# Kernel tuning notes

Measured on AMD Instinct MI355X. Metric: run time of the kernel, lower is better.

## Reference

```python
import jax, jax.numpy as jnp
import numpy as np

OBS_DIM = 512
ACT_DIM = 32
HIDDEN_DIM = 1024
MSG_DIM = 128
POS_EM_DIM = 128
T = 256


def pos_table(n, dim):
    pos = np.arange(n)[:, None].astype(np.float64)
    j = np.arange(dim)[None, :]
    tab = pos / np.power(10000.0, 2 * (j // 2) / dim)
    tab[:, 0::2] = np.sin(tab[:, 0::2])
    tab[:, 1::2] = np.cos(tab[:, 1::2])
    return tab.astype(np.float32)


def setup_inputs() -> dict:
    key = jax.random.key(0)
    ks = jax.random.split(key, 12)
    in_dim = 1 + ACT_DIM
    s = 0.1
    return {
        "obs": jax.random.normal(ks[0], (T, OBS_DIM), jnp.float32),
        "prev_act": jax.random.normal(ks[1], (T, ACT_DIM), jnp.float32),
        "in_shift": jnp.zeros((OBS_DIM,), jnp.float32),
        "in_scale": jnp.ones((OBS_DIM,), jnp.float32),
        "pos_embedding": jnp.asarray(pos_table(HIDDEN_DIM, POS_EM_DIM)),
        "W_ih": s * jax.random.normal(ks[2], (4 * POS_EM_DIM, in_dim), jnp.float32),
        "b_ih": s * jax.random.normal(ks[3], (4 * POS_EM_DIM,), jnp.float32),
        "W_hh": s * jax.random.normal(ks[4], (4 * POS_EM_DIM, POS_EM_DIM), jnp.float32),
        "b_hh": s * jax.random.normal(ks[5], (4 * POS_EM_DIM,), jnp.float32),
        "Wq": s * jax.random.normal(ks[6], (MSG_DIM, POS_EM_DIM), jnp.float32),
        "bq": s * jax.random.normal(ks[7], (MSG_DIM,), jnp.float32),
        "Wk": s * jax.random.normal(ks[8], (MSG_DIM, POS_EM_DIM), jnp.float32),
        "bk": s * jax.random.normal(ks[9], (MSG_DIM,), jnp.float32),
    }


def reference(obs, prev_act, in_shift, in_scale, pos_embedding,
              W_ih, b_ih, W_hh, b_hh, Wq, bq, Wk, bk):
    # input normalization (buffers default to identity)
    x = (obs - in_shift) / (in_scale + 1e-8)  # (T, obs_dim)
    # query projection of the positional table is constant across steps
    q = pos_embedding @ Wq.T + bq             # (hidden_dim, msg_dim)
    inv_scale = 1.0 / jnp.sqrt(jnp.float32(MSG_DIM))

    def step(carry, inp):
        h, c = carry                            # (obs_dim, pos_em_dim) each
        s, a = inp                              # (obs_dim,), (act_dim,)
        # state-action pair: each obs scalar paired with the full prev action
        xa = jnp.concatenate(
            [s[:, None], jnp.broadcast_to(a, (OBS_DIM, ACT_DIM))], axis=-1)
        gates = xa @ W_ih.T + b_ih + h @ W_hh.T + b_hh
        i, f, g, o = jnp.split(gates, 4, axis=-1)  # torch LSTMCell gate order
        c = jax.nn.sigmoid(f) * c + jax.nn.sigmoid(i) * jnp.tanh(g)
        h = jax.nn.sigmoid(o) * jnp.tanh(c)
        k = h @ Wk.T + bk                       # (obs_dim, msg_dim)
        w = jnp.tanh((q @ k.T) * inv_scale)     # (hidden_dim, obs_dim)
        out = w @ s                             # (hidden_dim,)
        return (h, c), out

    h0 = jnp.zeros((OBS_DIM, POS_EM_DIM), x.dtype)
    c0 = jnp.zeros_like(h0)
    _, outs = jax.lax.scan(step, (h0, c0), (x, prev_act))
    return jnp.tanh(outs)                       # (T, hidden_dim)
```

## Files before the change

### kernel.cpp

```cpp
#include <hip/hip_runtime.h>
#include <hip/hip_fp16.h>

#define T_STEPS 256
#define OBS 512
#define ACT 32
#define HID 1024
#define PED 128
#define MSG 128
#define GATES 512
#define HSTR 136
#define L1 1.4426950408889634f
#define L2C 2.8853900817779268f
#define QSCALE 0.2550348805576823f

typedef _Float16 half8  __attribute__((ext_vector_type(8)));
typedef float    floatx4 __attribute__((ext_vector_type(4)));

__device__ __forceinline__ float fast_exp2(float x) { return __builtin_amdgcn_exp2f(x); }
__device__ __forceinline__ float fast_rcp(float x)  { return __builtin_amdgcn_rcpf(x); }
__device__ __forceinline__ float tanh_f(float x) {
    return fmaf(-2.0f, fast_rcp(fast_exp2(2.8853900817779268f * x) + 1.0f), 1.0f);
}

__global__ void k_pre(const float* __restrict__ obs, const float* __restrict__ act,
                      const float* __restrict__ shift, const float* __restrict__ scale,
                      const float* __restrict__ W_ih, const float* __restrict__ b_ih,
                      const float* __restrict__ b_hh,
                      float* __restrict__ xnorm, float* __restrict__ apre_p) {
    int t = blockIdx.x;
    int tid = threadIdx.x;
    __shared__ float a_s[ACT];
    if (tid < ACT) a_s[tid] = act[t * ACT + tid];
    __syncthreads();
    for (int n = tid; n < OBS; n += 256) {
        xnorm[t * OBS + n] = (obs[t * OBS + n] - shift[n]) / (scale[n] + 1e-8f);
    }
    for (int j = tid; j < GATES; j += 256) {
        float acc = b_ih[j] + b_hh[j];
        const float* wr = W_ih + j * 33 + 1;
#pragma unroll
        for (int u = 0; u < ACT; ++u) acc = fmaf(a_s[u], wr[u], acc);
        int g = j >> 7, p = j & 127;
        apre_p[t * GATES + p * 4 + g] = acc;
    }
}

__global__ void k_qproj(const float* __restrict__ pe, const float* __restrict__ Wq,
                        const float* __restrict__ bq, const float* __restrict__ Wk,
                        const float* __restrict__ bk,
                        _Float16* __restrict__ qh, float* __restrict__ cb) {
    int m = blockIdx.x;
    int d = threadIdx.x;
    __shared__ float pe_s[PED];
    __shared__ float q_s[PED];
    __shared__ float red_s[2];
    pe_s[d] = pe[m * PED + d];
    __syncthreads();
    const float* wr = Wq + d * PED;
    float a = bq[d];
#pragma unroll 8
    for (int p = 0; p < PED; ++p) a = fmaf(pe_s[p], wr[p], a);
    q_s[d] = a;
    float pb = a * bk[d];
#pragma unroll
    for (int off = 32; off; off >>= 1) pb += __shfl_xor(pb, off, 64);
    if ((d & 63) == 0) red_s[d >> 6] = pb;
    __syncthreads();
    float acc = 0.f;
#pragma unroll 8
    for (int p = 0; p < PED; ++p) acc = fmaf(q_s[p], Wk[p * PED + d], acc);
    qh[m * PED + d] = (_Float16)(acc * QSCALE);
    if (d == 0) cb[m] = (red_s[0] + red_s[1]) * QSCALE;
}

__global__ __launch_bounds__(512, 1)
void k_lstm(const float* __restrict__ xnorm, const float* __restrict__ apre_p,
            const float* __restrict__ W_ih, const float* __restrict__ W_hh,
            _Float16* __restrict__ H16) {
    const int tid = threadIdx.x;
    const int lane = tid & 63, wv = tid >> 6;
    const int l15 = lane & 15, quad = lane >> 4;
    const int n0 = blockIdx.x * 4;
    const int p = 16 * wv + l15;

    half8 bfr[4][4];
    float wih0[4];
#pragma unroll
    for (int g = 0; g < 4; ++g) {
        const int col = 128 * g + p;
        const float* wrow = W_hh + (size_t)col * PED;
#pragma unroll
        for (int c = 0; c < 4; ++c) {
            const int k0 = c * 32 + quad * 8;
            float4 f0 = *(const float4*)(wrow + k0);
            float4 f1 = *(const float4*)(wrow + k0 + 4);
            bfr[g][c] = (half8){(_Float16)f0.x, (_Float16)f0.y, (_Float16)f0.z, (_Float16)f0.w,
                                (_Float16)f1.x, (_Float16)f1.y, (_Float16)f1.z, (_Float16)f1.w};
        }
        wih0[g] = W_ih[(size_t)col * 33];
    }

    __shared__ _Float16 h_s[2][16 * HSTR];
    __shared__ float x_s[T_STEPS * 4];

    for (int idx = tid; idx < T_STEPS * 4; idx += 512)
        x_s[idx] = xnorm[(idx >> 2) * OBS + n0 + (idx & 3)];
    for (int idx = tid; idx < 2 * 16 * HSTR; idx += 512)
        ((_Float16*)h_s)[idx] = (_Float16)0.f;

    float c0 = 0.f;
    const float* apl = apre_p + p * 4;
    float4 ap = *(const float4*)(apl);
    __syncthreads();

    _Float16* Hg = H16 + (size_t)(n0 + quad) * MSG + p;
    int buf = 0;
    for (int t = 0; t < T_STEPS; ++t) {
        half8 af[4];
        const _Float16* hb = h_s[buf] + l15 * HSTR + quad * 8;
#pragma unroll
        for (int c = 0; c < 4; ++c) af[c] = *(const half8*)(hb + c * 32);

        floatx4 acc[4];
        acc[0] = (floatx4){ap.x, ap.x, ap.x, ap.x};
        acc[1] = (floatx4){ap.y, ap.y, ap.y, ap.y};
        acc[2] = (floatx4){ap.z, ap.z, ap.z, ap.z};
        acc[3] = (floatx4){ap.w, ap.w, ap.w, ap.w};
#pragma unroll
        for (int g = 0; g < 4; ++g)
#pragma unroll
            for (int c = 0; c < 4; ++c)
                acc[g] = __builtin_amdgcn_mfma_f32_16x16x32_f16(
                    af[c], bfr[g][c], acc[g], 0, 0, 0);

        const int tn = (t + 1 < T_STEPS) ? t + 1 : t;
        float4 ap_n = *(const float4*)(apl + tn * GATES);

        const float x = x_s[t * 4 + quad];
        float gi = fmaf(x, wih0[0], acc[0][0]);
        float gf = fmaf(x, wih0[1], acc[1][0]);
        float gg = fmaf(x, wih0[2], acc[2][0]);
        float go = fmaf(x, wih0[3], acc[3][0]);

        float Di = 1.f + fast_exp2(fminf(-L1 * gi, 20.f));
        float Df = 1.f + fast_exp2(fminf(-L1 * gf, 20.f));
        float Dg = 1.f + fast_exp2(fminf(L2C * gg, 20.f));
        float DfDg = Df * Dg, DiDg = Di * Dg, DiDf = Di * Df;
        float r3 = fast_rcp(Di * DfDg);
        float iDi = r3 * DfDg, iDf = r3 * DiDg, iDg = r3 * DiDf;
        float cn = fmaf(iDf, c0, iDi * fmaf(-2.f, iDg, 1.f));
        c0 = cn;
        float Do = 1.f + fast_exp2(fminf(-L1 * go, 20.f));
        float Dc = 1.f + fast_exp2(fminf(L2C * cn, 20.f));
        float r2 = fast_rcp(Do * Dc);
        float iDo = r2 * Dc, iDc = r2 * Do;
        _Float16 hq = (_Float16)(iDo * fmaf(-2.f, iDc, 1.f));

        h_s[buf ^ 1][(4 * quad) * HSTR + p] = hq;
        Hg[0] = hq;
        Hg += OBS * MSG;

        ap = ap_n;
        buf ^= 1;
        __syncthreads();
    }
}

__global__ __launch_bounds__(256, 4)
void k_attn(const _Float16* __restrict__ qh, const float* __restrict__ cb,
            const _Float16* __restrict__ H16, const float* __restrict__ xnorm,
            float* __restrict__ outp) {
    const int t = blockIdx.x >> 3;
    const int mq = blockIdx.x & 7;
    const int tid = threadIdx.x;
    const int lane = tid & 63, wave = tid >> 6;
    const int l15 = lane & 15, quad = lane >> 4;
    const int m0 = mq * 128 + wave * 32;

    half8 afrag[2][4];
    floatx4 cbv[2];
#pragma unroll
    for (int mt = 0; mt < 2; ++mt) {
        const half8* qrow = (const half8*)(qh + (size_t)(m0 + mt * 16 + l15) * PED);
#pragma unroll
        for (int c = 0; c < 4; ++c) afrag[mt][c] = qrow[c * 4 + quad];
        cbv[mt] = *(const floatx4*)(cb + m0 + mt * 16 + quad * 4);
    }

    float outacc[8];
#pragma unroll
    for (int i = 0; i < 8; ++i) outacc[i] = 0.f;

    const _Float16* Hb = H16 + (size_t)t * (OBS * MSG) + (size_t)l15 * MSG + quad * 8;
    const float* xb = xnorm + t * OBS + l15;

    half8 bf[4];
    float sv;
#pragma unroll
    for (int c = 0; c < 4; ++c) bf[c] = *(const half8*)(Hb + c * 32);
    sv = xb[0];

    for (int nt = 0; nt < 32; ++nt) {
        half8 bfn[4];
        float svn = 0.f;
        if (nt < 31) {
            const _Float16* Hn = Hb + (nt + 1) * (16 * MSG);
#pragma unroll
            for (int c = 0; c < 4; ++c) bfn[c] = *(const half8*)(Hn + c * 32);
            svn = xb[(nt + 1) * 16];
        }

        floatx4 acc[2];
#pragma unroll
        for (int mt = 0; mt < 2; ++mt) {
            acc[mt] = cbv[mt];
#pragma unroll
            for (int c = 0; c < 4; ++c)
                acc[mt] = __builtin_amdgcn_mfma_f32_16x16x32_f16(
                    afrag[mt][c], bf[c], acc[mt], 0, 0, 0);
        }

#pragma unroll
        for (int mt = 0; mt < 2; ++mt) {
            float E0 = fast_exp2(fminf(acc[mt][0], 20.f));
            float E1 = fast_exp2(fminf(acc[mt][1], 20.f));
            float E2 = fast_exp2(fminf(acc[mt][2], 20.f));
            float E3 = fast_exp2(fminf(acc[mt][3], 20.f));
            float D0 = 1.f + E0, D1 = 1.f + E1, D2 = 1.f + E2, D3 = 1.f + E3;
            float m01 = D0 * D1, m23 = D2 * D3;
            float rp = fast_rcp(m01 * m23);
            float rA = rp * m23, rB = rp * m01;
            float i0 = rA * D1, i1 = rA * D0, i2 = rB * D3, i3 = rB * D2;
            outacc[mt * 4 + 0] = fmaf(fmaf(-2.f, i0, 1.f), sv, outacc[mt * 4 + 0]);
            outacc[mt * 4 + 1] = fmaf(fmaf(-2.f, i1, 1.f), sv, outacc[mt * 4 + 1]);
            outacc[mt * 4 + 2] = fmaf(fmaf(-2.f, i2, 1.f), sv, outacc[mt * 4 + 2]);
            outacc[mt * 4 + 3] = fmaf(fmaf(-2.f, i3, 1.f), sv, outacc[mt * 4 + 3]);
        }

#pragma unroll
        for (int c = 0; c < 4; ++c) bf[c] = bfn[c];
        sv = svn;
    }

#pragma unroll
    for (int i = 0; i < 8; ++i) {
        float v = outacc[i];
        v += __shfl_xor(v, 1, 16);
        v += __shfl_xor(v, 2, 16);
        v += __shfl_xor(v, 4, 16);
        v += __shfl_xor(v, 8, 16);
        outacc[i] = v;
    }
    if (l15 == 0) {
        const int mbase = m0 + quad * 4;
#pragma unroll
        for (int mt = 0; mt < 2; ++mt)
#pragma unroll
            for (int r = 0; r < 4; ++r)
                outp[(size_t)t * HID + mbase + mt * 16 + r] = tanh_f(outacc[mt * 4 + r]);
    }
}

extern "C" void kernel_launch(void* const* d_in, const int* in_sizes, int n_in,
                              void* d_out, int out_size, void* d_ws, size_t ws_size,
                              hipStream_t stream) {
    const float* obs      = (const float*)d_in[0];
    const float* prev_act = (const float*)d_in[1];
    const float* in_shift = (const float*)d_in[2];
    const float* in_scale = (const float*)d_in[3];
    const float* pos_emb  = (const float*)d_in[4];
    const float* W_ih     = (const float*)d_in[5];
    const float* b_ih     = (const float*)d_in[6];
    const float* W_hh     = (const float*)d_in[7];
    const float* b_hh     = (const float*)d_in[8];
    const float* Wq       = (const float*)d_in[9];
    const float* bq       = (const float*)d_in[10];
    const float* Wk       = (const float*)d_in[11];
    const float* bk       = (const float*)d_in[12];
    float* outp = (float*)d_out;

    float* ws = (float*)d_ws;
    float* xnorm  = ws;
    float* apre_p = ws + 131072;
    _Float16* qh  = (_Float16*)(ws + 262144);
    float* cbuf   = ws + 327680;
    _Float16* H16 = (_Float16*)(ws + 328704);

    k_pre<<<T_STEPS, 256, 0, stream>>>(obs, prev_act, in_shift, in_scale,
                                       W_ih, b_ih, b_hh, xnorm, apre_p);
    k_qproj<<<HID, 128, 0, stream>>>(pos_emb, Wq, bq, Wk, bk, qh, cbuf);
    k_lstm<<<128, 512, 0, stream>>>(xnorm, apre_p, W_ih, W_hh, H16);
    k_attn<<<T_STEPS * 8, 256, 0, stream>>>(qh, cbuf, H16, xnorm, outp);
}
```

Baseline: 365.8 us.

## Stage key tiles in shared memory and remap block index in attention kernel

```diff
diff --git a/kernel.cpp b/kernel.cpp
--- a/kernel.cpp
+++ b/kernel.cpp
@@ -9,6 +9,7 @@
 #define MSG 128
 #define GATES 512
 #define HSTR 136
+#define KSTR 17
 #define L1 1.4426950408889634f
 #define L2C 2.8853900817779268f
 #define QSCALE 0.2550348805576823f
@@ -170,8 +171,8 @@
 void k_attn(const _Float16* __restrict__ qh, const float* __restrict__ cb,
             const _Float16* __restrict__ H16, const float* __restrict__ xnorm,
             float* __restrict__ outp) {
-    const int t = blockIdx.x >> 3;
-    const int mq = blockIdx.x & 7;
+    const int t = blockIdx.x & 255;
+    const int mq = blockIdx.x >> 8;
     const int tid = threadIdx.x;
     const int lane = tid & 63, wave = tid >> 6;
     const int l15 = lane & 15, quad = lane >> 4;
@@ -187,59 +188,71 @@
         cbv[mt] = *(const floatx4*)(cb + m0 + mt * 16 + quad * 4);
     }
 
+    __shared__ half8 kbuf[64 * KSTR];
+    __shared__ float s_s[64];
+
     float outacc[8];
 #pragma unroll
     for (int i = 0; i < 8; ++i) outacc[i] = 0.f;
 
-    const _Float16* Hb = H16 + (size_t)t * (OBS * MSG) + (size_t)l15 * MSG + quad * 8;
-    const float* xb = xnorm + t * OBS + l15;
-
-    half8 bf[4];
-    float sv;
-#pragma unroll
-    for (int c = 0; c < 4; ++c) bf[c] = *(const half8*)(Hb + c * 32);
-    sv = xb[0];
-
-    for (int nt = 0; nt < 32; ++nt) {
-        half8 bfn[4];
-        float svn = 0.f;
-        if (nt < 31) {
-            const _Float16* Hn = Hb + (nt + 1) * (16 * MSG);
-#pragma unroll
-            for (int c = 0; c < 4; ++c) bfn[c] = *(const half8*)(Hn + c * 32);
-            svn = xb[(nt + 1) * 16];
+    const half8* Ht = (const half8*)(H16 + (size_t)t * (OBS * MSG));
+    half8 pf[4];
+    float sf = 0.f;
+#pragma unroll
+    for (int i = 0; i < 4; ++i) pf[i] = Ht[i * 256 + tid];
+    if (tid < 64) sf = xnorm[t * OBS + tid];
+
+    for (int ch = 0; ch < 8; ++ch) {
+        __syncthreads();
+#pragma unroll
+        for (int i = 0; i < 4; ++i) {
+            int f = i * 256 + tid;
+            kbuf[(f >> 4) * KSTR + (f & 15)] = pf[i];
         }
-
-        floatx4 acc[2];
-#pragma unroll
-        for (int mt = 0; mt < 2; ++mt) {
-            acc[mt] = cbv[mt];
+        if (tid < 64) s_s[tid] = sf;
+        __syncthreads();
+        if (ch < 7) {
+            const half8* Hn = Ht + (ch + 1) * 1024;
+#pragma unroll
+            for (int i = 0; i < 4; ++i) pf[i] = Hn[i * 256 + tid];
+            if (tid < 64) sf = xnorm[t * OBS + (ch + 1) * 64 + tid];
+        }
+
+#pragma unroll
+        for (int nt = 0; nt < 4; ++nt) {
+            half8 bfrag[4];
 #pragma unroll
             for (int c = 0; c < 4; ++c)
-                acc[mt] = __builtin_amdgcn_mfma_f32_16x16x32_f16(
-                    afrag[mt][c], bf[c], acc[mt], 0, 0, 0);
+                bfrag[c] = kbuf[(nt * 16 + l15) * KSTR + c * 4 + quad];
+
+            floatx4 acc[2];
+#pragma unroll
+            for (int mt = 0; mt < 2; ++mt) {
+                acc[mt] = cbv[mt];
+#pragma unroll
+                for (int c = 0; c < 4; ++c)
+                    acc[mt] = __builtin_amdgcn_mfma_f32_16x16x32_f16(
+                        afrag[mt][c], bfrag[c], acc[mt], 0, 0, 0);
+            }
+
+            const float sv = s_s[nt * 16 + l15];
+#pragma unroll
+            for (int mt = 0; mt < 2; ++mt) {
+                float E0 = fast_exp2(fminf(acc[mt][0], 20.f));
+                float E1 = fast_exp2(fminf(acc[mt][1], 20.f));
+                float E2 = fast_exp2(fminf(acc[mt][2], 20.f));
+                float E3 = fast_exp2(fminf(acc[mt][3], 20.f));
+                float D0 = 1.f + E0, D1 = 1.f + E1, D2 = 1.f + E2, D3 = 1.f + E3;
+                float m01 = D0 * D1, m23 = D2 * D3;
+                float rp = fast_rcp(m01 * m23);
+                float rA = rp * m23, rB = rp * m01;
+                float i0 = rA * D1, i1 = rA * D0, i2 = rB * D3, i3 = rB * D2;
+                outacc[mt * 4 + 0] = fmaf(fmaf(-2.f, i0, 1.f), sv, outacc[mt * 4 + 0]);
+                outacc[mt * 4 + 1] = fmaf(fmaf(-2.f, i1, 1.f), sv, outacc[mt * 4 + 1]);
+                outacc[mt * 4 + 2] = fmaf(fmaf(-2.f, i2, 1.f), sv, outacc[mt * 4 + 2]);
+                outacc[mt * 4 + 3] = fmaf(fmaf(-2.f, i3, 1.f), sv, outacc[mt * 4 + 3]);
+            }
         }
-
-#pragma unroll
-        for (int mt = 0; mt < 2; ++mt) {
-            float E0 = fast_exp2(fminf(acc[mt][0], 20.f));
-            float E1 = fast_exp2(fminf(acc[mt][1], 20.f));
-            float E2 = fast_exp2(fminf(acc[mt][2], 20.f));
-            float E3 = fast_exp2(fminf(acc[mt][3], 20.f));
-            float D0 = 1.f + E0, D1 = 1.f + E1, D2 = 1.f + E2, D3 = 1.f + E3;
-            float m01 = D0 * D1, m23 = D2 * D3;
-            float rp = fast_rcp(m01 * m23);
-            float rA = rp * m23, rB = rp * m01;
-            float i0 = rA * D1, i1 = rA * D0, i2 = rB * D3, i3 = rB * D2;
-            outacc[mt * 4 + 0] = fmaf(fmaf(-2.f, i0, 1.f), sv, outacc[mt * 4 + 0]);
-            outacc[mt * 4 + 1] = fmaf(fmaf(-2.f, i1, 1.f), sv, outacc[mt * 4 + 1]);
-            outacc[mt * 4 + 2] = fmaf(fmaf(-2.f, i2, 1.f), sv, outacc[mt * 4 + 2]);
-            outacc[mt * 4 + 3] = fmaf(fmaf(-2.f, i3, 1.f), sv, outacc[mt * 4 + 3]);
-        }
-
-#pragma unroll
-        for (int c = 0; c < 4; ++c) bf[c] = bfn[c];
-        sv = svn;
     }
 
 #pragma unroll
```

Measured after the change: 300.6 us. -17.8%, faster.
